# Kernel optimization log

Measured on AMD Instinct MI355X. Metric: run time of the kernel, lower is better.

## Reference

```python
import jax, jax.numpy as jnp
import numpy as np

H = 8
DK = 32  # head_dim = 256 // 8
SCALE = 1.0 / np.float32(np.sqrt(DK))
EPS = 1e-5


def _ln(x, g, b):
    mu = jnp.mean(x, axis=-1, keepdims=True)
    var = jnp.var(x, axis=-1, keepdims=True)
    return (x - mu) / jnp.sqrt(var + EPS) * g + b


def _lin(x, W, b):
    return x @ W + b


def setup_inputs() -> dict:
    key = jax.random.key(0)
    ks = jax.random.split(key, 16)
    B, M, N, D, F = 4, 64, 512, 256, 1024
    s = 0.02
    inp = {
        "machine_emb": jax.random.normal(ks[0], (B, M, D), jnp.float32),
        "op_emb": jax.random.normal(ks[1], (B, N, D), jnp.float32),
        "edge_emb": jax.random.normal(ks[2], (B, N, M, D), jnp.float32),
        "o2m_mask": jax.random.bernoulli(ks[3], 0.3, (B, N, M)),
    }
    # projection weights stored as (in, out)
    for i, nm in enumerate(["q", "k", "v", "o", "ks", "vs", "e"]):
        inp["W" + nm] = jax.random.normal(ks[4 + i], (D, D), jnp.float32) * s
        inp["b" + nm] = jnp.zeros((D,), jnp.float32)
    # layernorms: norm1 (g1/b1), norm2 (g2/b2), norm_op (gop/bop)
    for nm in ["1", "2", "op"]:
        inp["g" + nm] = jnp.ones((D,), jnp.float32)
        inp["bn" + nm] = jnp.zeros((D,), jnp.float32)
    # FFN
    inp["Wf1"] = jax.random.normal(ks[11], (D, F), jnp.float32) * s
    inp["bf1"] = jnp.zeros((F,), jnp.float32)
    inp["Wf2"] = jax.random.normal(ks[12], (F, D), jnp.float32) * s
    inp["bf2"] = jnp.zeros((D,), jnp.float32)
    return inp


def reference(machine_emb, op_emb, edge_emb, o2m_mask,
              Wq, bq, Wk, bk, Wv, bv, Wo, bo, Wks, bks, Wvs, bvs, We, be,
              g1, bn1, g2, bn2, gop, bnop, Wf1, bf1, Wf2, bf2):
    B, M, D = machine_emb.shape
    N = op_emb.shape[1]

    residual = machine_emb
    machine_norm = _ln(machine_emb, g1, bn1)
    op_norm = _ln(op_emb, gop, bnop)

    # (B, H, M, dk) / (B, H, N, dk)
    q_m = _lin(machine_norm, Wq, bq).reshape(B, M, H, DK).transpose(0, 2, 1, 3)
    k_o = _lin(op_norm, Wk, bk).reshape(B, N, H, DK).transpose(0, 2, 1, 3)
    v_o = _lin(op_norm, Wv, bv).reshape(B, N, H, DK).transpose(0, 2, 1, 3)

    # edge: (B,N,M,D) -> (B,H,M,N,dk)
    edge = _lin(edge_emb, We, be).reshape(B, N, M, H, DK)
    edge = edge.transpose(0, 3, 2, 1, 4)  # bhmnd

    q_total = q_m[:, :, :, None, :] + edge          # (B,H,M,N,dk)
    k_total = k_o[:, :, None, :, :] + edge          # (B,H,M,N,dk)
    v_total = v_o[:, :, None, :, :] + edge          # (B,H,M,N,dk)

    scores = jnp.sum(q_total * k_total, axis=-1) * SCALE  # (B,H,M,N)

    k_self = _lin(machine_norm, Wks, bks).reshape(B, M, H, DK).transpose(0, 2, 1, 3)
    self_scores = jnp.sum(q_m * k_self, axis=-1) * SCALE   # (B,H,M)

    cross_mask = o2m_mask.transpose(0, 2, 1)[:, None, :, :]  # (B,1,M,N)
    combined_scores = jnp.concatenate([self_scores[..., None], scores], axis=-1)  # (B,H,M,1+N)
    self_flag = jnp.ones((B, 1, M, 1), dtype=bool)
    combined_mask = jnp.concatenate([self_flag, jnp.broadcast_to(cross_mask, (B, 1, M, N))], axis=-1)
    combined_scores = jnp.where(combined_mask, combined_scores, -jnp.inf)

    attn = jax.nn.softmax(combined_scores, axis=-1)
    attn = jnp.where(jnp.isnan(attn), 0.0, attn)

    v_self = _lin(machine_norm, Wvs, bvs).reshape(B, M, H, DK).transpose(0, 2, 1, 3)
    combined_values = jnp.concatenate([v_self[:, :, :, None, :], v_total], axis=3)  # (B,H,M,1+N,dk)

    attn_out = jnp.einsum('bhmi,bhmid->bhmd', attn, combined_values)
    attn_out = attn_out.transpose(0, 2, 1, 3).reshape(B, M, D)
    attn_out = _lin(attn_out, Wo, bo)

    machine_emb = residual + attn_out
    h = _ln(machine_emb, g2, bn2)
    ffn = _lin(jax.nn.relu(_lin(h, Wf1, bf1)), Wf2, bf2)
    return machine_emb + ffn
```

## Files before the change

kernel.cpp:

```cpp
#include <hip/hip_runtime.h>
#include <hip/hip_bf16.h>
#include <math.h>

#define H_ 8
#define DK_ 32
#define B_ 4
#define M_ 64
#define N_ 512
#define D_ 256
#define F_ 1024

static constexpr float SCALE = 0.17677669529663687f;
static constexpr float EPS = 1e-5f;

typedef __bf16 bf16x8 __attribute__((ext_vector_type(8)));
typedef float f32x4 __attribute__((ext_vector_type(4)));

__device__ inline float bfbits2f(unsigned int b) {
    union { unsigned int i; float f; } c; c.i = b << 16; return c.f;
}
__device__ inline void unpack8(uint4 u, float* f) {
    f[0] = bfbits2f(u.x & 0xffffu); f[1] = bfbits2f(u.x >> 16);
    f[2] = bfbits2f(u.y & 0xffffu); f[3] = bfbits2f(u.y >> 16);
    f[4] = bfbits2f(u.z & 0xffffu); f[5] = bfbits2f(u.z >> 16);
    f[6] = bfbits2f(u.w & 0xffffu); f[7] = bfbits2f(u.w >> 16);
}

struct TTArgs {
    const void* src[9];
    void* dst[9];
    int tcum[9];
    int kl[9];
    int nl[9];
    const float* bq; const float* bks; const float* bvs; const float* bk; const float* bv;
    float* bqksvs; float* bkv; int* flags;
};

__global__ __launch_bounds__(256) void prep_all(TTArgs a) {
    __shared__ float ld[64][65];
    int bx = blockIdx.x;
    int t = threadIdx.x;
    if (bx >= a.tcum[8]) {
        a.bqksvs[t] = a.bq[t];
        a.bqksvs[256 + t] = a.bks[t];
        a.bqksvs[512 + t] = a.bvs[t];
        a.bkv[t] = a.bk[t];
        a.bkv[256 + t] = a.bv[t];
        if (t == 0) a.flags[1] = 0;
        return;
    }
    int ti = 0;
    while (bx >= a.tcum[ti]) ti++;
    int j = bx - (ti ? a.tcum[ti - 1] : 0);
    int K = 1 << a.kl[ti], N = 1 << a.nl[ti];
    int ntn = N >> 6;
    int kt = j / ntn, nt = j - kt * ntn;
    const float* src = (const float*)a.src[ti];
    __hip_bfloat16* dst = (__hip_bfloat16*)a.dst[ti];
    int col = t & 63, r0 = t >> 6;
#pragma unroll
    for (int i = 0; i < 16; ++i) {
        int r = i * 4 + r0;
        ld[r][col] = src[(size_t)(kt * 64 + r) * N + nt * 64 + col];
    }
    __syncthreads();
#pragma unroll
    for (int i = 0; i < 16; ++i) {
        int r = i * 4 + r0;
        dst[(size_t)(nt * 64 + r) * K + kt * 64 + col] = __float2bfloat16(ld[col][r]);
    }
}

__device__ inline float block_reduce256(float v, bool is_max, float* sbuf) {
#pragma unroll
    for (int off = 32; off > 0; off >>= 1) {
        float o = __shfl_down(v, off, 64);
        v = is_max ? fmaxf(v, o) : (v + o);
    }
    int lane = threadIdx.x & 63, wid = threadIdx.x >> 6;
    if (lane == 0) sbuf[wid] = v;
    __syncthreads();
    float r;
    if (is_max) r = fmaxf(fmaxf(sbuf[0], sbuf[1]), fmaxf(sbuf[2], sbuf[3]));
    else        r = sbuf[0] + sbuf[1] + sbuf[2] + sbuf[3];
    __syncthreads();
    return r;
}

__global__ __launch_bounds__(256) void ln_detect(const float* __restrict__ me,
                                                 const float* __restrict__ oe,
                                                 const float* __restrict__ g1v,
                                                 const float* __restrict__ b1v,
                                                 const float* __restrict__ gov,
                                                 const float* __restrict__ bov,
                                                 __hip_bfloat16* __restrict__ mnorm,
                                                 __hip_bfloat16* __restrict__ onorm,
                                                 const unsigned int* __restrict__ mask,
                                                 int* __restrict__ flags) {
    __shared__ float sbuf[4];
    int bx = blockIdx.x, t = threadIdx.x;
    if (bx >= 2304) {
        uint4 v = ((const uint4*)mask)[(size_t)(bx - 2304) * 256 + t];
        if (v.x > 1u || v.y > 1u || v.z > 1u || v.w > 1u) atomicOr(flags + 1, 1);
        return;
    }
    const float* xin; const float* g; const float* bta; __hip_bfloat16* out; int row;
    if (bx < 256) { xin = me; g = g1v; bta = b1v; out = mnorm; row = bx; }
    else          { xin = oe; g = gov; bta = bov; out = onorm; row = bx - 256; }
    size_t idx = (size_t)row * 256 + t;
    float x = xin[idx];
    float s  = block_reduce256(x, false, sbuf);
    float ss = block_reduce256(x * x, false, sbuf);
    float mu = s * (1.f / 256.f);
    float var = ss * (1.f / 256.f) - mu * mu;
    float y = (x - mu) * rsqrtf(var + EPS) * g[t] + bta[t];
    out[idx] = __float2bfloat16(y);
}

__global__ __launch_bounds__(256) void ln_kernel(const float* __restrict__ xin,
                                                 const float* __restrict__ g,
                                                 const float* __restrict__ bta,
                                                 __hip_bfloat16* __restrict__ out) {
    __shared__ float sbuf[4];
    int row = blockIdx.x, d = threadIdx.x;
    size_t idx = (size_t)row * 256 + d;
    float x = xin[idx];
    float s  = block_reduce256(x, false, sbuf);
    float ss = block_reduce256(x * x, false, sbuf);
    float mu = s * (1.f / 256.f);
    float var = ss * (1.f / 256.f) - mu * mu;
    float y = (x - mu) * rsqrtf(var + EPS) * g[d] + bta[d];
    out[idx] = __float2bfloat16(y);
}

__global__ __launch_bounds__(256) void gemm64(const __hip_bfloat16* __restrict__ A,
                                              const __hip_bfloat16* __restrict__ BT,
                                              const float* __restrict__ bias,
                                              const float* __restrict__ resid,
                                              void* __restrict__ out,
                                              int K, int ldc, int flags) {
    __shared__ __align__(16) __bf16 As[64 * 40];
    __shared__ __align__(16) __bf16 Bs[64 * 40];
    const int rowBase = blockIdx.x * 64;
    const int colBase = blockIdx.y * 64;
    const int t = threadIdx.x;
    const int w = t >> 6;
    const int l = t & 63;
    const int lrow = l & 15;
    const int lk8 = (l >> 4) * 8;
    const int ar = t >> 2;
    const int ac = (t & 3) * 8;

    f32x4 acc[4] = {};
    for (int k0 = 0; k0 < K; k0 += 32) {
        bf16x8 av = *(const bf16x8*)(A + (size_t)(rowBase + ar) * K + k0 + ac);
        bf16x8 bv = *(const bf16x8*)(BT + (size_t)(colBase + ar) * K + k0 + ac);
        __syncthreads();
        *(bf16x8*)(As + ar * 40 + ac) = av;
        *(bf16x8*)(Bs + ar * 40 + ac) = bv;
        __syncthreads();
        bf16x8 af = *(const bf16x8*)(As + (w * 16 + lrow) * 40 + lk8);
#pragma unroll
        for (int c = 0; c < 4; ++c) {
            bf16x8 bf = *(const bf16x8*)(Bs + (c * 16 + lrow) * 40 + lk8);
            acc[c] = __builtin_amdgcn_mfma_f32_16x16x32_bf16(af, bf, acc[c], 0, 0, 0);
        }
    }
    int rbase = rowBase + w * 16 + ((l >> 4) * 4);
#pragma unroll
    for (int c = 0; c < 4; ++c) {
        int col = colBase + c * 16 + (l & 15);
        float bb = bias[col];
#pragma unroll
        for (int r = 0; r < 4; ++r) {
            int row = rbase + r;
            size_t oi = (size_t)row * ldc + col;
            float v = acc[c][r] + bb;
            if (flags & 1) v = fmaxf(v, 0.f);
            if (flags & 4) v += resid[oi];
            if (flags & 8) ((float*)out)[oi] = v;
            else ((__hip_bfloat16*)out)[oi] = __float2bfloat16(v);
        }
    }
}

__global__ __launch_bounds__(256) void gemm64_dual(const __hip_bfloat16* __restrict__ A0,
                                                   const __hip_bfloat16* __restrict__ BT0,
                                                   const float* __restrict__ bias0,
                                                   __hip_bfloat16* __restrict__ out0,
                                                   const __hip_bfloat16* __restrict__ A1,
                                                   const __hip_bfloat16* __restrict__ BT1,
                                                   const float* __restrict__ bias1,
                                                   __hip_bfloat16* __restrict__ out1) {
    __shared__ __align__(16) __bf16 As[64 * 40];
    __shared__ __align__(16) __bf16 Bs[64 * 40];
    const int id = blockIdx.x;
    const __hip_bfloat16* A; const __hip_bfloat16* BT; const float* bias;
    __hip_bfloat16* out; int bx, by, ldc;
    if (id < 48) { A = A0; BT = BT0; bias = bias0; out = out0; bx = id & 3;  by = id >> 2; ldc = 768; }
    else { int j = id - 48; A = A1; BT = BT1; bias = bias1; out = out1; bx = j & 31; by = j >> 5; ldc = 512; }
    const int rowBase = bx * 64;
    const int colBase = by * 64;
    const int t = threadIdx.x;
    const int w = t >> 6;
    const int l = t & 63;
    const int lrow = l & 15;
    const int lk8 = (l >> 4) * 8;
    const int ar = t >> 2;
    const int ac = (t & 3) * 8;

    f32x4 acc[4] = {};
    for (int k0 = 0; k0 < 256; k0 += 32) {
        bf16x8 av = *(const bf16x8*)(A + (size_t)(rowBase + ar) * 256 + k0 + ac);
        bf16x8 bv = *(const bf16x8*)(BT + (size_t)(colBase + ar) * 256 + k0 + ac);
        __syncthreads();
        *(bf16x8*)(As + ar * 40 + ac) = av;
        *(bf16x8*)(Bs + ar * 40 + ac) = bv;
        __syncthreads();
        bf16x8 af = *(const bf16x8*)(As + (w * 16 + lrow) * 40 + lk8);
#pragma unroll
        for (int c = 0; c < 4; ++c) {
            bf16x8 bf = *(const bf16x8*)(Bs + (c * 16 + lrow) * 40 + lk8);
            acc[c] = __builtin_amdgcn_mfma_f32_16x16x32_bf16(af, bf, acc[c], 0, 0, 0);
        }
    }
    int rbase = rowBase + w * 16 + ((l >> 4) * 4);
#pragma unroll
    for (int c = 0; c < 4; ++c) {
        int col = colBase + c * 16 + (l & 15);
        float bb = bias[col];
#pragma unroll
        for (int r = 0; r < 4; ++r) {
            int row = rbase + r;
            out[(size_t)row * ldc + col] = __float2bfloat16(acc[c][r] + bb);
        }
    }
}

__global__ __launch_bounds__(256) void edge_gemm4(const float* __restrict__ E,
                                                  const __hip_bfloat16* __restrict__ WeT,
                                                  const float* __restrict__ be,
                                                  const __hip_bfloat16* __restrict__ qkvs,
                                                  const __hip_bfloat16* __restrict__ kov,
                                                  const void* __restrict__ mask,
                                                  const int* __restrict__ flags,
                                                  __hip_bfloat16* __restrict__ eperm,
                                                  float* __restrict__ scT) {
    __shared__ __align__(16) __bf16 smem[64 * 272];
    __bf16* As = smem;
    __bf16* Cs = smem;
    const int bn = blockIdx.x;
    const int b = bn >> 9, n = bn & 511;
    const int t = threadIdx.x;
    const int w = t >> 6;
    const int l = t & 63;
    const int lrow = l & 15;
    const int lk8 = (l >> 4) * 8;
    const int ar = t >> 2;
    const int ac = (t & 3) * 8;
    const float* Ab = E + (size_t)bn * 64 * 256;

    f32x4 acc[4][4] = {};
    for (int k0 = 0; k0 < 256; k0 += 32) {
        const float* ap = Ab + (size_t)ar * 256 + k0 + ac;
        float4 x0 = *(const float4*)ap;
        float4 x1 = *(const float4*)(ap + 4);
        bf16x8 av;
        av[0] = (__bf16)x0.x; av[1] = (__bf16)x0.y; av[2] = (__bf16)x0.z; av[3] = (__bf16)x0.w;
        av[4] = (__bf16)x1.x; av[5] = (__bf16)x1.y; av[6] = (__bf16)x1.z; av[7] = (__bf16)x1.w;
        __syncthreads();
        *(bf16x8*)(As + ar * 40 + ac) = av;
        __syncthreads();
        bf16x8 af[4];
#pragma unroll
        for (int rr = 0; rr < 4; ++rr)
            af[rr] = *(const bf16x8*)(As + (rr * 16 + lrow) * 40 + lk8);
#pragma unroll
        for (int c = 0; c < 4; ++c) {
            bf16x8 bf = *(const bf16x8*)(WeT + (size_t)(w * 64 + c * 16 + lrow) * 256 + k0 + lk8);
#pragma unroll
            for (int rr = 0; rr < 4; ++rr)
                acc[rr][c] = __builtin_amdgcn_mfma_f32_16x16x32_bf16(af[rr], bf, acc[rr][c], 0, 0, 0);
        }
    }
    __syncthreads();
#pragma unroll
    for (int c = 0; c < 4; ++c) {
        int col = w * 64 + c * 16 + (l & 15);
        float bb = be[col];
#pragma unroll
        for (int rr = 0; rr < 4; ++rr) {
#pragma unroll
            for (int r = 0; r < 4; ++r) {
                int m = rr * 16 + (l >> 4) * 4 + r;
                Cs[m * 272 + col] = (__bf16)(acc[rr][c][r] + bb);
            }
        }
    }
    __syncthreads();
    const bool u8 = flags[1] != 0;
    const int seg = t & 31;
    const int h = seg >> 2;
    const int dk8 = (seg & 3) * 8;
#pragma unroll
    for (int j = 0; j < 8; ++j) {
        int m = j * 8 + (t >> 5);
        uint4 ev4 = *(const uint4*)(Cs + m * 272 + seg * 8);
        size_t bhm = (size_t)((b * 8 + h) * 64 + m);
        *(uint4*)(eperm + (bhm * 512 + n) * 32 + dk8) = ev4;
        float ev[8], qf[8], kf[8];
        unpack8(ev4, ev);
        uint4 qv4 = *(const uint4*)(qkvs + (size_t)(b * 64 + m) * 768 + h * 32 + dk8);
        uint4 kv4 = *(const uint4*)(kov + (size_t)(b * 512 + n) * 512 + h * 32 + dk8);
        unpack8(qv4, qf);
        unpack8(kv4, kf);
        float p = 0.f;
#pragma unroll
        for (int i = 0; i < 8; ++i)
            p += (qf[i] + ev[i]) * (kf[i] + ev[i]);
        p += __shfl_xor(p, 1, 64);
        p += __shfl_xor(p, 2, 64);
        if ((t & 3) == 0) {
            int mi = (b * 512 + n) * 64 + m;
            int mk = u8 ? (int)((const unsigned char*)mask)[mi] : ((const int*)mask)[mi];
            scT[(bhm << 9) + n] = mk ? p * SCALE : -__builtin_inff();
        }
    }
}

__global__ __launch_bounds__(256) void smax_attnout(const float* __restrict__ sc,
                                                    const __hip_bfloat16* __restrict__ qkvs,
                                                    const __hip_bfloat16* __restrict__ kov,
                                                    const __hip_bfloat16* __restrict__ eperm,
                                                    __hip_bfloat16* __restrict__ AO) {
    __shared__ float sbuf[4];
    __shared__ float attnS[512];
    __shared__ float selfSc;
    __shared__ float selfA;
    __shared__ float red[16][8];
    int bhm = blockIdx.x;
    int m = bhm & 63;
    int h = (bhm >> 6) & 7;
    int b = bhm >> 9;
    int t = threadIdx.x;
    if (t == 0) {
        const __hip_bfloat16* q  = qkvs + (size_t)(b * 64 + m) * 768 + h * 32;
        const __hip_bfloat16* ks = q + 256;
        float s = 0.f;
        for (int i = 0; i < 32; ++i) s += __bfloat162float(q[i]) * __bfloat162float(ks[i]);
        selfSc = s * SCALE;
    }
    __syncthreads();
    float sv = selfSc;
    float s0 = sc[(size_t)bhm * 512 + t];
    float s1 = sc[(size_t)bhm * 512 + 256 + t];
    float mx = block_reduce256(fmaxf(fmaxf(s0, s1), sv), true, sbuf);
    float e0 = __expf(s0 - mx);
    float e1 = __expf(s1 - mx);
    float eself = __expf(sv - mx);
    float sum = block_reduce256(e0 + e1 + (t == 0 ? eself : 0.f), false, sbuf);
    float inv = 1.f / sum;
    attnS[t] = e0 * inv;
    attnS[256 + t] = e1 * inv;
    if (t == 0) selfA = eself * inv;
    __syncthreads();

    const int d8 = (t & 3) * 8;
    const int ng = t >> 2;
    const int w = t >> 6, l = t & 63;
    const __hip_bfloat16* ebase = eperm + (size_t)bhm * 512 * 32;
    const __hip_bfloat16* vbase = kov + (size_t)(b * 512) * 512 + 256 + h * 32;
    float accv[8] = {};
#pragma unroll
    for (int i = 0; i < 8; ++i) {
        int n = ng + i * 64;
        float a = attnS[n];
        float ev[8], vv[8];
        uint4 e4 = *(const uint4*)(ebase + (size_t)n * 32 + d8);
        uint4 v4 = *(const uint4*)(vbase + (size_t)n * 512 + d8);
        unpack8(e4, ev);
        unpack8(v4, vv);
#pragma unroll
        for (int k = 0; k < 8; ++k) accv[k] += a * (vv[k] + ev[k]);
    }
#pragma unroll
    for (int off = 4; off <= 32; off <<= 1) {
#pragma unroll
        for (int k = 0; k < 8; ++k) accv[k] += __shfl_xor(accv[k], off, 64);
    }
    if ((l >> 2) == 0) {
#pragma unroll
        for (int k = 0; k < 8; ++k) red[w * 4 + (l & 3)][k] = accv[k];
    }
    __syncthreads();
    if (t < 32) {
        int slot = t >> 3, elem = t & 7;
        float r = red[slot][elem] + red[4 + slot][elem] + red[8 + slot][elem] + red[12 + slot][elem];
        float vs = __bfloat162float(qkvs[(size_t)(b * 64 + m) * 768 + 512 + h * 32 + t]);
        r += selfA * vs;
        AO[(size_t)(b * 64 + m) * 256 + h * 32 + t] = __float2bfloat16(r);
    }
}

extern "C" void kernel_launch(void* const* d_in, const int* in_sizes, int n_in,
                              void* d_out, int out_size, void* d_ws, size_t ws_size,
                              hipStream_t stream) {
    const float* machine_emb = (const float*)d_in[0];
    const float* op_emb      = (const float*)d_in[1];
    const float* edge_emb    = (const float*)d_in[2];
    const void*  o2m_mask    = d_in[3];

    char* p = (char*)d_ws;
    int* flags = (int*)p;                        p += 256;
    __hip_bfloat16* WqksvsT = (__hip_bfloat16*)p; p += 196608 * 2;
    __hip_bfloat16* WkvT    = (__hip_bfloat16*)p; p += 131072 * 2;
    __hip_bfloat16* WoT     = (__hip_bfloat16*)p; p += 65536 * 2;
    __hip_bfloat16* WeT     = (__hip_bfloat16*)p; p += 65536 * 2;
    __hip_bfloat16* Wf1T    = (__hip_bfloat16*)p; p += 262144 * 2;
    __hip_bfloat16* Wf2T    = (__hip_bfloat16*)p; p += 262144 * 2;
    float* bqksvs           = (float*)p;          p += 768 * 4;
    float* bkv              = (float*)p;          p += 512 * 4;
    __hip_bfloat16* mnorm   = (__hip_bfloat16*)p; p += 65536 * 2;
    __hip_bfloat16* onorm   = (__hip_bfloat16*)p; p += 524288 * 2;
    __hip_bfloat16* qkvs    = (__hip_bfloat16*)p; p += 196608 * 2;
    __hip_bfloat16* kov     = (__hip_bfloat16*)p; p += 1048576 * 2;
    __hip_bfloat16* eperm   = (__hip_bfloat16*)p; p += (size_t)33554432 * 2;
    float* scT       = (float*)p;                p += (size_t)1048576 * 4;
    __hip_bfloat16* AO = (__hip_bfloat16*)p;     p += 65536 * 2;
    float* m2        = (float*)p;                p += 65536 * 4;
    __hip_bfloat16* hn = (__hip_bfloat16*)p;     p += 65536 * 2;
    __hip_bfloat16* h1 = (__hip_bfloat16*)p;     p += 262144 * 2;

    TTArgs ta;
    const int srcIdx[9] = {4, 12, 14, 6, 8, 10, 16, 24, 26};
    void* dsts[9] = {WqksvsT, WqksvsT + 65536, WqksvsT + 131072,
                     WkvT, WkvT + 65536, WoT, WeT, Wf1T, Wf2T};
    const int kl9[9] = {8, 8, 8, 8, 8, 8, 8, 8, 10};
    const int nl9[9] = {8, 8, 8, 8, 8, 8, 8, 10, 8};
    int tcum = 0;
    for (int i = 0; i < 9; ++i) {
        ta.src[i] = d_in[srcIdx[i]];
        ta.dst[i] = dsts[i];
        int tiles = (1 << (kl9[i] - 6)) * (1 << (nl9[i] - 6));
        tcum += tiles;
        ta.tcum[i] = tcum;
        ta.kl[i] = kl9[i];
        ta.nl[i] = nl9[i];
    }
    ta.bq = (const float*)d_in[5];  ta.bks = (const float*)d_in[13];
    ta.bvs = (const float*)d_in[15]; ta.bk = (const float*)d_in[7];
    ta.bv = (const float*)d_in[9];
    ta.bqksvs = bqksvs; ta.bkv = bkv; ta.flags = flags;

    hipLaunchKernelGGL(prep_all, dim3(tcum + 1), dim3(256), 0, stream, ta);

    hipLaunchKernelGGL(ln_detect, dim3(2336), dim3(256), 0, stream,
                       machine_emb, op_emb,
                       (const float*)d_in[18], (const float*)d_in[19],
                       (const float*)d_in[22], (const float*)d_in[23],
                       mnorm, onorm, (const unsigned int*)o2m_mask, flags);

    hipLaunchKernelGGL(gemm64_dual, dim3(304), dim3(256), 0, stream,
                       mnorm, WqksvsT, bqksvs, qkvs,
                       onorm, WkvT, bkv, kov);

    hipLaunchKernelGGL(edge_gemm4, dim3(2048), dim3(256), 0, stream,
                       edge_emb, WeT, (const float*)d_in[17],
                       qkvs, kov, o2m_mask, flags, eperm, scT);

    hipLaunchKernelGGL(smax_attnout, dim3(2048), dim3(256), 0, stream,
                       scT, qkvs, kov, eperm, AO);

    hipLaunchKernelGGL(gemm64, dim3(4, 4), dim3(256), 0, stream,
                       AO, WoT, (const float*)d_in[11], machine_emb, m2, 256, 256, 4 | 8);
    hipLaunchKernelGGL(ln_kernel, dim3(256), dim3(256), 0, stream,
                       m2, (const float*)d_in[20], (const float*)d_in[21], hn);
    hipLaunchKernelGGL(gemm64, dim3(4, 16), dim3(256), 0, stream,
                       hn, Wf1T, (const float*)d_in[25], nullptr, h1, 256, 1024, 1);
    hipLaunchKernelGGL(gemm64, dim3(4, 4), dim3(256), 0, stream,
                       h1, Wf2T, (const float*)d_in[27], m2, (float*)d_out, 1024, 256, 4 | 8);
}
```

Before: 356.2 us.

## Fuse output projection with LayerNorm and fuse both FFN layers per row

Replaces the MFMA output-projection GEMM and separate LayerNorm with one per-row kernel that computes the projection, residual add and LayerNorm together. The two FFN GEMMs become a single 1024-thread per-row kernel that keeps the hidden activation in shared memory. This removes two launches and the h1 round trip through global memory. In exchange it uses scalar FMA instead of matrix cores, and every block rereads the full weight matrices.

Measured after the change: 361.4 us. No clear change (+1.5%).

```diff
diff --git a/kernel.cpp b/kernel.cpp
--- a/kernel.cpp
+++ b/kernel.cpp
@@ -115,73 +115,6 @@
     float var = ss * (1.f / 256.f) - mu * mu;
     float y = (x - mu) * rsqrtf(var + EPS) * g[t] + bta[t];
     out[idx] = __float2bfloat16(y);
-}
-
-__global__ __launch_bounds__(256) void ln_kernel(const float* __restrict__ xin,
-                                                 const float* __restrict__ g,
-                                                 const float* __restrict__ bta,
-                                                 __hip_bfloat16* __restrict__ out) {
-    __shared__ float sbuf[4];
-    int row = blockIdx.x, d = threadIdx.x;
-    size_t idx = (size_t)row * 256 + d;
-    float x = xin[idx];
-    float s  = block_reduce256(x, false, sbuf);
-    float ss = block_reduce256(x * x, false, sbuf);
-    float mu = s * (1.f / 256.f);
-    float var = ss * (1.f / 256.f) - mu * mu;
-    float y = (x - mu) * rsqrtf(var + EPS) * g[d] + bta[d];
-    out[idx] = __float2bfloat16(y);
-}
-
-__global__ __launch_bounds__(256) void gemm64(const __hip_bfloat16* __restrict__ A,
-                                              const __hip_bfloat16* __restrict__ BT,
-                                              const float* __restrict__ bias,
-                                              const float* __restrict__ resid,
-                                              void* __restrict__ out,
-                                              int K, int ldc, int flags) {
-    __shared__ __align__(16) __bf16 As[64 * 40];
-    __shared__ __align__(16) __bf16 Bs[64 * 40];
-    const int rowBase = blockIdx.x * 64;
-    const int colBase = blockIdx.y * 64;
-    const int t = threadIdx.x;
-    const int w = t >> 6;
-    const int l = t & 63;
-    const int lrow = l & 15;
-    const int lk8 = (l >> 4) * 8;
-    const int ar = t >> 2;
-    const int ac = (t & 3) * 8;
-
-    f32x4 acc[4] = {};
-    for (int k0 = 0; k0 < K; k0 += 32) {
-        bf16x8 av = *(const bf16x8*)(A + (size_t)(rowBase + ar) * K + k0 + ac);
-        bf16x8 bv = *(const bf16x8*)(BT + (size_t)(colBase + ar) * K + k0 + ac);
-        __syncthreads();
-        *(bf16x8*)(As + ar * 40 + ac) = av;
-        *(bf16x8*)(Bs + ar * 40 + ac) = bv;
-        __syncthreads();
-        bf16x8 af = *(const bf16x8*)(As + (w * 16 + lrow) * 40 + lk8);
-#pragma unroll
-        for (int c = 0; c < 4; ++c) {
-            bf16x8 bf = *(const bf16x8*)(Bs + (c * 16 + lrow) * 40 + lk8);
-            acc[c] = __builtin_amdgcn_mfma_f32_16x16x32_bf16(af, bf, acc[c], 0, 0, 0);
-        }
-    }
-    int rbase = rowBase + w * 16 + ((l >> 4) * 4);
-#pragma unroll
-    for (int c = 0; c < 4; ++c) {
-        int col = colBase + c * 16 + (l & 15);
-        float bb = bias[col];
-#pragma unroll
-        for (int r = 0; r < 4; ++r) {
-            int row = rbase + r;
-            size_t oi = (size_t)row * ldc + col;
-            float v = acc[c][r] + bb;
-            if (flags & 1) v = fmaxf(v, 0.f);
-            if (flags & 4) v += resid[oi];
-            if (flags & 8) ((float*)out)[oi] = v;
-            else ((__hip_bfloat16*)out)[oi] = __float2bfloat16(v);
-        }
-    }
 }
 
 __global__ __launch_bounds__(256) void gemm64_dual(const __hip_bfloat16* __restrict__ A0,
@@ -402,6 +335,85 @@
     }
 }
 
+__global__ __launch_bounds__(256) void oproj_ln(const __hip_bfloat16* __restrict__ AO,
+                                                const __hip_bfloat16* __restrict__ WoT,
+                                                const float* __restrict__ bo,
+                                                const float* __restrict__ resid,
+                                                const float* __restrict__ g2,
+                                                const float* __restrict__ bn2,
+                                                float* __restrict__ m2,
+                                                __hip_bfloat16* __restrict__ hn) {
+    __shared__ float rowA[256];
+    __shared__ float sbuf[4];
+    const int r = blockIdx.x;
+    const int t = threadIdx.x;
+    rowA[t] = __bfloat162float(AO[(size_t)r * 256 + t]);
+    __syncthreads();
+    float acc = 0.f;
+    const __hip_bfloat16* wrow = WoT + (size_t)t * 256;
+#pragma unroll
+    for (int k0 = 0; k0 < 256; k0 += 8) {
+        float wv[8];
+        unpack8(*(const uint4*)(wrow + k0), wv);
+#pragma unroll
+        for (int i = 0; i < 8; ++i) acc += rowA[k0 + i] * wv[i];
+    }
+    float v = acc + bo[t] + resid[(size_t)r * 256 + t];
+    m2[(size_t)r * 256 + t] = v;
+    float s  = block_reduce256(v, false, sbuf);
+    float ss = block_reduce256(v * v, false, sbuf);
+    float mu = s * (1.f / 256.f);
+    float var = ss * (1.f / 256.f) - mu * mu;
+    float y = (v - mu) * rsqrtf(var + EPS) * g2[t] + bn2[t];
+    hn[(size_t)r * 256 + t] = __float2bfloat16(y);
+}
+
+__global__ __launch_bounds__(1024) void ffn_fused(const __hip_bfloat16* __restrict__ hn,
+                                                  const __hip_bfloat16* __restrict__ Wf1T,
+                                                  const float* __restrict__ bf1,
+                                                  const __hip_bfloat16* __restrict__ Wf2T,
+                                                  const float* __restrict__ bf2,
+                                                  const float* __restrict__ m2,
+                                                  float* __restrict__ out) {
+    __shared__ float rowA[256];
+    __shared__ float hrow[4][260];
+    const int r = blockIdx.x;
+    const int t = threadIdx.x;
+    if (t < 256) rowA[t] = __bfloat162float(hn[(size_t)r * 256 + t]);
+    __syncthreads();
+    {
+        float acc = 0.f;
+        const __hip_bfloat16* wrow = Wf1T + (size_t)t * 256;
+#pragma unroll
+        for (int k0 = 0; k0 < 256; k0 += 8) {
+            float wv[8];
+            unpack8(*(const uint4*)(wrow + k0), wv);
+#pragma unroll
+            for (int i = 0; i < 8; ++i) acc += rowA[k0 + i] * wv[i];
+        }
+        hrow[t >> 8][t & 255] = fmaxf(acc + bf1[t], 0.f);
+    }
+    __syncthreads();
+    {
+        const int c = t >> 2;
+        const int kq = t & 3;
+        float acc = 0.f;
+        const __hip_bfloat16* wrow = Wf2T + (size_t)c * 1024 + kq * 256;
+        const float* hq = hrow[kq];
+#pragma unroll
+        for (int k0 = 0; k0 < 256; k0 += 8) {
+            float wv[8];
+            unpack8(*(const uint4*)(wrow + k0), wv);
+#pragma unroll
+            for (int i = 0; i < 8; ++i) acc += hq[k0 + i] * wv[i];
+        }
+        acc += __shfl_xor(acc, 1, 64);
+        acc += __shfl_xor(acc, 2, 64);
+        if (kq == 0)
+            out[(size_t)r * 256 + c] = m2[(size_t)r * 256 + c] + bf2[c] + acc;
+    }
+}
+
 extern "C" void kernel_launch(void* const* d_in, const int* in_sizes, int n_in,
                               void* d_out, int out_size, void* d_ws, size_t ws_size,
                               hipStream_t stream) {
@@ -429,7 +441,6 @@
     __hip_bfloat16* AO = (__hip_bfloat16*)p;     p += 65536 * 2;
     float* m2        = (float*)p;                p += 65536 * 4;
     __hip_bfloat16* hn = (__hip_bfloat16*)p;     p += 65536 * 2;
-    __hip_bfloat16* h1 = (__hip_bfloat16*)p;     p += 262144 * 2;
 
     TTArgs ta;
     const int srcIdx[9] = {4, 12, 14, 6, 8, 10, 16, 24, 26};
@@ -471,12 +482,11 @@
     hipLaunchKernelGGL(smax_attnout, dim3(2048), dim3(256), 0, stream,
                        scT, qkvs, kov, eperm, AO);
 
-    hipLaunchKernelGGL(gemm64, dim3(4, 4), dim3(256), 0, stream,
-                       AO, WoT, (const float*)d_in[11], machine_emb, m2, 256, 256, 4 | 8);
-    hipLaunchKernelGGL(ln_kernel, dim3(256), dim3(256), 0, stream,
-                       m2, (const float*)d_in[20], (const float*)d_in[21], hn);
-    hipLaunchKernelGGL(gemm64, dim3(4, 16), dim3(256), 0, stream,
-                       hn, Wf1T, (const float*)d_in[25], nullptr, h1, 256, 1024, 1);
-    hipLaunchKernelGGL(gemm64, dim3(4, 4), dim3(256), 0, stream,
-                       h1, Wf2T, (const float*)d_in[27], m2, (float*)d_out, 1024, 256, 4 | 8);
-}
+    hipLaunchKernelGGL(oproj_ln, dim3(256), dim3(256), 0, stream,
+                       AO, WoT, (const float*)d_in[11], machine_emb,
+                       (const float*)d_in[20], (const float*)d_in[21], m2, hn);
+
+    hipLaunchKernelGGL(ffn_fused, dim3(256), dim3(1024), 0, stream,
+                       hn, Wf1T, (const float*)d_in[25],
+                       Wf2T, (const float*)d_in[27], m2, (float*)d_out);
+}
```
